# Kernel tuning notes

Hardware: AMD Instinct MI355X
Metric: run time of the kernel (lower is better)

The kernel has to match this reference:

```python
import jax, jax.numpy as jnp
import numpy as np

B, S, D, H = 2, 2048, 1024, 16
A = D // H
NEG = -1e9


def setup_inputs() -> dict:
    key = jax.random.key(0)
    ks = jax.random.split(key, 5)
    std = 1.0 / np.sqrt(D)
    query = jax.random.normal(ks[0], (B, S, D), dtype=jnp.float32)
    context = jax.random.normal(ks[1], (B, S, D), dtype=jnp.float32)
    Wq = jax.random.normal(ks[2], (D, D), dtype=jnp.float32) * std
    Wkv = jax.random.normal(ks[3], (2 * D, D), dtype=jnp.float32) * std
    Wout = jax.random.normal(ks[4], (D, D), dtype=jnp.float32) * std
    # 2D additive causal mask [q_len, c_len]; module broadcasts it over batch and heads
    mask = jnp.where(jnp.tril(jnp.ones((S, S), dtype=bool)), 0.0, NEG).astype(jnp.float32)
    return {"query": query, "context": context, "Wq": Wq, "Wkv": Wkv, "Wout": Wout, "mask": mask}


def reference(query, context, Wq, Wkv, Wout, mask):
    b, q_len, d = query.shape
    c_len = context.shape[1]
    h, a = H, A
    scale = 1.0 / np.sqrt(d)  # NOTE: module scales by 1/sqrt(hidden_dim), not head dim

    q = query @ Wq.T                      # [b, q, d]
    kv = context @ Wkv.T                  # [b, c, 2d]
    k, v = jnp.split(kv, 2, axis=-1)

    q = q.reshape(b, q_len, h, a)
    k = k.reshape(b, c_len, h, a)
    v = v.reshape(b, c_len, h, a)

    scores = jnp.einsum('bqha,bkha->bqkh', q, k)      # [b, q, k, h]
    scores = scores + mask[None, :, :, None]          # mask added BEFORE scaling (faithful)
    attn = jax.nn.softmax(scores * scale, axis=2)     # softmax over key dim
    out = jnp.einsum('bqkh,bkha->bqha', attn, v).reshape(b, q_len, d)
    return out @ Wout.T
```

## Files before the change

### kernel.cpp

```cpp
#include <hip/hip_runtime.h>
#include <hip/hip_bf16.h>
#include <stdint.h>

#define S_LEN 2048
#define DIM   1024
#define NH    16
#define HD    64
#define BATCH 2

typedef __attribute__((ext_vector_type(4))) float f32x4;
typedef __attribute__((ext_vector_type(16))) float f32x16;
typedef __attribute__((ext_vector_type(8))) short bf16x8;
typedef __attribute__((ext_vector_type(4))) int i32x4;
typedef __hip_bfloat16 bf16;

__device__ inline void gload_lds16(const void* g, void* l) {
  __builtin_amdgcn_global_load_lds(
      (const __attribute__((address_space(1))) void*)g,
      (__attribute__((address_space(3))) void*)l, 16, 0, 0);
}

__device__ inline bf16x8 as_bf16x8(i32x4 x) {
  union { i32x4 i; bf16x8 v; } u; u.i = x; return u.v;
}
__device__ inline int cvt_pk_bf16(float lo, float hi) {
  int r;
  asm("v_cvt_pk_bf16_f32 %0, %1, %2" : "=v"(r) : "v"(lo), "v"(hi));
  return r;
}

__global__ __launch_bounds__(256) void cvt_all(
    const float* __restrict__ q, const float* __restrict__ c,
    const float* __restrict__ wq, const float* __restrict__ wkv,
    const float* __restrict__ wo,
    bf16* __restrict__ oq, bf16* __restrict__ oc, bf16* __restrict__ owq,
    bf16* __restrict__ owkv, bf16* __restrict__ owo) {
  const int N0 = 1048576, N1 = 1048576, N2 = 262144, N3 = 524288, N4 = 262144;
  const int total = N0 + N1 + N2 + N3 + N4;
  for (int i = blockIdx.x * 256 + threadIdx.x; i < total; i += gridDim.x * 256) {
    const float* src; bf16* dst; int off = i;
    if (i < N0)                { src = q;   dst = oq; }
    else if (i < N0 + N1)      { src = c;   dst = oc;   off -= N0; }
    else if (i < N0 + N1 + N2) { src = wq;  dst = owq;  off -= N0 + N1; }
    else if (i < N0 + N1 + N2 + N3) { src = wkv; dst = owkv; off -= N0 + N1 + N2; }
    else                       { src = wo;  dst = owo;  off -= N0 + N1 + N2 + N3; }
    float4 v = ((const float4*)src)[off];
    bf16 b0 = __float2bfloat16(v.x), b1 = __float2bfloat16(v.y);
    bf16 b2 = __float2bfloat16(v.z), b3 = __float2bfloat16(v.w);
    ushort4 o;
    o.x = *(unsigned short*)&b0; o.y = *(unsigned short*)&b1;
    o.z = *(unsigned short*)&b2; o.w = *(unsigned short*)&b3;
    ((ushort4*)dst)[off] = o;
  }
}

__device__ inline void gemm128_body(const bf16* __restrict__ A, const bf16* __restrict__ B,
                                    bf16* __restrict__ C, int N, int K, float alpha,
                                    int bm, int bn, bf16* Als, bf16* Bls) {
  const int tid = threadIdx.x;
  const int lane = tid & 63, wid = tid >> 6;
  const int wr = wid >> 1, wc = wid & 1;
  const int fr = lane & 15, fq = lane >> 4;

  f32x4 acc[4][4] = {};
  const int kTiles = K >> 5;
  for (int kt = 0; kt < kTiles; ++kt) {
    const int k0 = kt << 5;
    __syncthreads();
#pragma unroll
    for (int j = 0; j < 2; ++j) {
      int ob = wid * 2048 + j * 1024;
      int o = ob + lane * 16;
      int r = o >> 6;
      int kk = (o & 63) >> 1;
      gload_lds16(A + (size_t)(bm + r) * K + k0 + kk, (char*)Als + ob);
      gload_lds16(B + (size_t)(bn + r) * K + k0 + kk, (char*)Bls + ob);
    }
    __syncthreads();
    bf16x8 af[4], bfr[4];
#pragma unroll
    for (int m = 0; m < 4; ++m)
      af[m] = *(const bf16x8*)(Als + (wr * 64 + m * 16 + fr) * 32 + fq * 8);
#pragma unroll
    for (int n = 0; n < 4; ++n)
      bfr[n] = *(const bf16x8*)(Bls + (wc * 64 + n * 16 + fr) * 32 + fq * 8);
#pragma unroll
    for (int m = 0; m < 4; ++m)
#pragma unroll
      for (int n = 0; n < 4; ++n)
        acc[m][n] = __builtin_amdgcn_mfma_f32_16x16x32_bf16(af[m], bfr[n], acc[m][n], 0, 0, 0);
  }
#pragma unroll
  for (int m = 0; m < 4; ++m)
#pragma unroll
    for (int n = 0; n < 4; ++n)
#pragma unroll
      for (int i = 0; i < 4; ++i) {
        int row = bm + wr * 64 + m * 16 + fq * 4 + i;
        int col = bn + wc * 64 + n * 16 + fr;
        C[(size_t)row * N + col] = __float2bfloat16(acc[m][n][i] * alpha);
      }
}

__global__ __launch_bounds__(256) void gemm_proj(
    const bf16* __restrict__ Aq, const bf16* __restrict__ Bq, bf16* __restrict__ Cq,
    const bf16* __restrict__ Akv, const bf16* __restrict__ Bkv, bf16* __restrict__ Ckv,
    float qalpha) {
  __shared__ __align__(16) bf16 Als[128 * 32];
  __shared__ __align__(16) bf16 Bls[128 * 32];
  const int bid = blockIdx.x;
  const bf16 *A, *B; bf16 *C; int N; float alpha; int bx, by;
  if (bid < 256) { A = Aq;  B = Bq;  C = Cq;  N = 1024; alpha = qalpha; bx = bid & 7;  by = bid >> 3; }
  else { int t = bid - 256; A = Akv; B = Bkv; C = Ckv; N = 2048; alpha = 1.0f; bx = t & 15; by = t >> 4; }
  gemm128_body(A, B, C, N, 1024, alpha, by * 128, bx * 128, Als, Bls);
}

__global__ __launch_bounds__(256) void gemm_bt_n64(
    const bf16* __restrict__ A, const bf16* __restrict__ B,
    float* __restrict__ C, int M, int N, int K) {
  __shared__ __align__(16) bf16 Als[128 * 32];
  __shared__ __align__(16) bf16 Bls[64 * 32];
  const int tid = threadIdx.x;
  const int lane = tid & 63, wid = tid >> 6;
  const int bm = blockIdx.y * 128, bn = blockIdx.x * 64;
  const int fr = lane & 15, fq = lane >> 4;

  f32x4 acc[2][4] = {};
  const int kTiles = K >> 5;
  for (int kt = 0; kt < kTiles; ++kt) {
    const int k0 = kt << 5;
    __syncthreads();
#pragma unroll
    for (int j = 0; j < 2; ++j) {
      int ob = wid * 2048 + j * 1024;
      int o = ob + lane * 16;
      int r = o >> 6;
      int kk = (o & 63) >> 1;
      gload_lds16(A + (size_t)(bm + r) * K + k0 + kk, (char*)Als + ob);
    }
    {
      int ob = wid * 1024;
      int o = ob + lane * 16;
      int r = o >> 6;
      int kk = (o & 63) >> 1;
      gload_lds16(B + (size_t)(bn + r) * K + k0 + kk, (char*)Bls + ob);
    }
    __syncthreads();
    bf16x8 af[2], bfr[4];
#pragma unroll
    for (int m = 0; m < 2; ++m)
      af[m] = *(const bf16x8*)(Als + (wid * 32 + m * 16 + fr) * 32 + fq * 8);
#pragma unroll
    for (int n = 0; n < 4; ++n)
      bfr[n] = *(const bf16x8*)(Bls + (n * 16 + fr) * 32 + fq * 8);
#pragma unroll
    for (int m = 0; m < 2; ++m)
#pragma unroll
      for (int n = 0; n < 4; ++n)
        acc[m][n] = __builtin_amdgcn_mfma_f32_16x16x32_bf16(af[m], bfr[n], acc[m][n], 0, 0, 0);
  }
#pragma unroll
  for (int m = 0; m < 2; ++m)
#pragma unroll
    for (int n = 0; n < 4; ++n)
#pragma unroll
      for (int i = 0; i < 4; ++i) {
        int row = bm + wid * 32 + m * 16 + fq * 4 + i;
        int col = bn + n * 16 + fr;
        C[(size_t)row * N + col] = acc[m][n][i];
      }
}

__global__ __launch_bounds__(256) void transpose_v(
    const bf16* __restrict__ KV, bf16* __restrict__ Vt) {
  __shared__ __align__(16) bf16 tile[64][72];
  const int t = threadIdx.x;
  const int s0 = blockIdx.x * 64, h = blockIdx.y, b = blockIdx.z;
#pragma unroll
  for (int j = 0; j < 2; ++j) {
    int s = j * 32 + (t >> 3);
    int a = (t & 7) * 8;
    bf16x8 v = *(const bf16x8*)(KV + (size_t)(b * S_LEN + s0 + s) * (2 * DIM) + DIM + h * HD + a);
    *(bf16x8*)&tile[s][a] = v;
  }
  __syncthreads();
#pragma unroll
  for (int j = 0; j < 2; ++j) {
    int a = j * 32 + (t >> 3);
    int sc = (t & 7) * 8;
    bf16x8 v;
#pragma unroll
    for (int e = 0; e < 8; ++e)
      ((short*)&v)[e] = *(const short*)&tile[sc + e][a];
    *(bf16x8*)(Vt + (size_t)((b * NH + h) * HD + a) * S_LEN + s0 + sc) = v;
  }
}

__global__ __launch_bounds__(256, 4) void attn_fwd(
    const bf16* __restrict__ Q,
    const bf16* __restrict__ KV,
    const bf16* __restrict__ Vt,
    bf16* __restrict__ O) {
  __shared__ __align__(16) bf16 Kls[3][64 * 64];
  __shared__ __align__(16) bf16 Vls[3][64 * 64];
  __shared__ float Rls[128];
  const int tid = threadIdx.x, lane = tid & 63, wid = tid >> 6;
  const int l31 = lane & 31, hi = lane >> 5;
  const int bid = blockIdx.x;
  const int qx = 15 - (bid >> 5);
  const int hb = bid & 31;
  const int h = hb >> 1, b = hb & 1;
  const int rw0 = qx * 128 + wid * 32;
  const int qrow = rw0 + l31;
  const float NEGINF = -__builtin_inff();

  bf16x8 qf[4];
#pragma unroll
  for (int ka = 0; ka < 4; ++ka)
    qf[ka] = *(const bf16x8*)(Q + (size_t)(b * S_LEN + qrow) * DIM + h * HD + ka * 16 + hi * 8);

  f32x16 oacc[2] = {};
  float rsum = 0.f;

  auto stage = [&](int buf, int kt) {
#pragma unroll
    for (int j = 0; j < 2; ++j) {
      int ob = (wid * 2 + j) * 1024;
      int o = ob + lane * 16;
      int r = o >> 7;
      int sb = (o & 127) ^ ((r & 7) << 4);
      gload_lds16(KV + (size_t)(b * S_LEN + kt * 64 + r) * (2 * DIM) + h * HD + (sb >> 1),
                  (char*)Kls[buf] + ob);
      gload_lds16(Vt + (size_t)((b * NH + h) * HD + r) * S_LEN + kt * 64 + (sb >> 1),
                  (char*)Vls[buf] + ob);
    }
  };

  const int nt = 2 * qx + 2;
  stage(0, 0);
  stage(1, 1 < nt ? 1 : 0);

  for (int kt = 0; kt < nt; ++kt) {
    if (kt + 1 < nt) asm volatile("s_waitcnt vmcnt(4)" ::: "memory");
    else             asm volatile("s_waitcnt vmcnt(0)" ::: "memory");
    __syncthreads();

    const int cb = kt % 3;
    if (64 * kt <= rw0 + 31) {
      const bf16* Kb = Kls[cb];
      const bf16* Vb = Vls[cb];
      const bool maskt = (64 * kt + 63 > rw0);

#pragma unroll
      for (int kb = 0; kb < 2; ++kb) {
        f32x16 c = {};
        __builtin_amdgcn_s_setprio(1);
#pragma unroll
        for (int ka = 0; ka < 4; ++ka) {
          int row = kb * 32 + l31;
          bf16x8 kf = *(const bf16x8*)((const char*)Kb + row * 128 +
                                       ((ka * 32 + hi * 16) ^ ((row & 7) << 4)));
          c = __builtin_amdgcn_mfma_f32_32x32x16_bf16(kf, qf[ka], c, 0, 0, 0);
        }
        __builtin_amdgcn_s_setprio(0);

        float pe[16];
        if (maskt) {
#pragma unroll
          for (int r = 0; r < 16; ++r) {
            int key = kt * 64 + kb * 32 + (r & 3) + 8 * (r >> 2) + 4 * hi;
            float s = (key <= qrow) ? c[r] : NEGINF;
            pe[r] = __builtin_amdgcn_exp2f(s);
            rsum += pe[r];
          }
        } else {
#pragma unroll
          for (int r = 0; r < 16; ++r) {
            pe[r] = __builtin_amdgcn_exp2f(c[r]);
            rsum += pe[r];
          }
        }

        int u[8], x[8];
#pragma unroll
        for (int t = 0; t < 8; ++t) u[t] = cvt_pk_bf16(pe[2 * t], pe[2 * t + 1]);
#pragma unroll
        for (int t = 0; t < 8; ++t) x[t] = __shfl_xor(u[t], 32);
        i32x4 w0, w1;
        w0[0] = hi ? x[2] : u[0]; w0[1] = hi ? x[3] : u[1];
        w0[2] = hi ? u[2] : x[0]; w0[3] = hi ? u[3] : x[1];
        w1[0] = hi ? x[6] : u[4]; w1[1] = hi ? x[7] : u[5];
        w1[2] = hi ? u[6] : x[4]; w1[3] = hi ? u[7] : x[5];
        bf16x8 pa0 = as_bf16x8(w0), pa1 = as_bf16x8(w1);

        __builtin_amdgcn_s_setprio(1);
#pragma unroll
        for (int pl = 0; pl < 2; ++pl) {
          bf16x8 pa = pl ? pa1 : pa0;
#pragma unroll
          for (int nb = 0; nb < 2; ++nb) {
            int a = nb * 32 + l31;
            bf16x8 vf = *(const bf16x8*)((const char*)Vb + a * 128 +
                                         ((kb * 64 + pl * 32 + hi * 16) ^ ((a & 7) << 4)));
            oacc[nb] = __builtin_amdgcn_mfma_f32_32x32x16_bf16(pa, vf, oacc[nb], 0, 0, 0);
          }
        }
        __builtin_amdgcn_s_setprio(0);
      }
    }

    if (kt + 2 < nt) stage((kt + 2) % 3, kt + 2);
  }

  rsum += __shfl_xor(rsum, 32);
  if (hi == 0) Rls[wid * 32 + l31] = 1.0f / rsum;
#pragma unroll
  for (int nb = 0; nb < 2; ++nb)
#pragma unroll
    for (int r = 0; r < 16; ++r) {
      int qloc = (r & 3) + 8 * (r >> 2) + 4 * hi;
      float rv = Rls[wid * 32 + qloc];
      int qg = rw0 + qloc;
      O[(size_t)(b * S_LEN + qg) * DIM + h * HD + nb * 32 + l31] =
          __float2bfloat16(oacc[nb][r] * rv);
    }
}

extern "C" void kernel_launch(void* const* d_in, const int* in_sizes, int n_in,
                              void* d_out, int out_size, void* d_ws, size_t ws_size,
                              hipStream_t stream) {
  (void)in_sizes; (void)n_in; (void)out_size; (void)ws_size;
  const float* query   = (const float*)d_in[0];
  const float* context = (const float*)d_in[1];
  const float* Wq      = (const float*)d_in[2];
  const float* Wkv     = (const float*)d_in[3];
  const float* Wout    = (const float*)d_in[4];
  float* out = (float*)d_out;

  bf16* ws = (bf16*)d_ws;
  const size_t nBSD = (size_t)BATCH * S_LEN * DIM;
  bf16* qbf    = ws;
  bf16* cbf    = qbf + nBSD;
  bf16* wqbf   = cbf + nBSD;
  bf16* wkvbf  = wqbf + (size_t)DIM * DIM;
  bf16* woutbf = wkvbf + (size_t)2 * DIM * DIM;
  bf16* Qp     = woutbf + (size_t)DIM * DIM;
  bf16* KVp    = Qp + nBSD;
  bf16* Vtp    = KVp + 2 * nBSD;
  bf16* Op     = Vtp + nBSD;

  cvt_all<<<2048, 256, 0, stream>>>(query, context, Wq, Wkv, Wout,
                                    qbf, cbf, wqbf, wkvbf, woutbf);

  gemm_proj<<<768, 256, 0, stream>>>(qbf, wqbf, Qp, cbf, wkvbf, KVp, 0.0450842200277801f);

  transpose_v<<<dim3(S_LEN / 64, NH, BATCH), 256, 0, stream>>>(KVp, Vtp);
  attn_fwd<<<512, 256, 0, stream>>>(Qp, KVp, Vtp, Op);
  const int M = BATCH * S_LEN;
  gemm_bt_n64<<<dim3(DIM / 64, M / 128), 256, 0, stream>>>(Op, woutbf, out, M, DIM, DIM);
}
```

Baseline: 126.9 us.

## Split attention key range across two blocks and combine partial outputs

Each causal query tile's key range is split into two halves handled by separate blocks, doubling the grid from 512 to 1024. Unnormalized partial outputs and row sums go to scratch buffers that reuse the already-consumed bf16 input workspace. A new combine kernel sums the two partials and normalizes. This targets load imbalance and low occupancy from the triangular workload, at the cost of an extra launch, extra global traffic, and an extra bf16 rounding of the partials.

```diff
diff --git a/kernel.cpp b/kernel.cpp
--- a/kernel.cpp
+++ b/kernel.cpp
@@ -27,6 +27,11 @@
   int r;
   asm("v_cvt_pk_bf16_f32 %0, %1, %2" : "=v"(r) : "v"(lo), "v"(hi));
   return r;
+}
+__device__ inline float b2f(short s) {
+  union { unsigned int u; float f; } w;
+  w.u = ((unsigned int)(unsigned short)s) << 16;
+  return w.f;
 }
 
 __global__ __launch_bounds__(256) void cvt_all(
@@ -200,27 +205,33 @@
     const bf16* __restrict__ Q,
     const bf16* __restrict__ KV,
     const bf16* __restrict__ Vt,
-    bf16* __restrict__ O) {
+    bf16* __restrict__ Opart,
+    float* __restrict__ Rpart) {
   __shared__ __align__(16) bf16 Kls[3][64 * 64];
   __shared__ __align__(16) bf16 Vls[3][64 * 64];
-  __shared__ float Rls[128];
   const int tid = threadIdx.x, lane = tid & 63, wid = tid >> 6;
   const int l31 = lane & 31, hi = lane >> 5;
   const int bid = blockIdx.x;
-  const int qx = 15 - (bid >> 5);
-  const int hb = bid & 31;
+  const int qx = 15 - (bid >> 6);
+  const int rem = bid & 63;
+  const int c = rem >> 5;
+  const int hb = rem & 31;
   const int h = hb >> 1, b = hb & 1;
   const int rw0 = qx * 128 + wid * 32;
   const int qrow = rw0 + l31;
   const float NEGINF = -__builtin_inff();
 
+  const int cnt = qx + 1;
+  const int kt0 = c * cnt;
+  const int p = ((b * NH + h) * 32) + qx * 2 + c;
+
   bf16x8 qf[4];
 #pragma unroll
   for (int ka = 0; ka < 4; ++ka)
     qf[ka] = *(const bf16x8*)(Q + (size_t)(b * S_LEN + qrow) * DIM + h * HD + ka * 16 + hi * 8);
 
   f32x16 oacc[2] = {};
-  float rsum = 0.f;
+  float rsA[4] = {0.f, 0.f, 0.f, 0.f};
 
   auto stage = [&](int buf, int kt) {
 #pragma unroll
@@ -236,16 +247,16 @@
     }
   };
 
-  const int nt = 2 * qx + 2;
-  stage(0, 0);
-  stage(1, 1 < nt ? 1 : 0);
-
-  for (int kt = 0; kt < nt; ++kt) {
-    if (kt + 1 < nt) asm volatile("s_waitcnt vmcnt(4)" ::: "memory");
+  stage(0, kt0);
+  if (cnt > 1) stage(1, kt0 + 1);
+
+  for (int i = 0; i < cnt; ++i) {
+    const int kt = kt0 + i;
+    if (i + 1 < cnt) asm volatile("s_waitcnt vmcnt(4)" ::: "memory");
     else             asm volatile("s_waitcnt vmcnt(0)" ::: "memory");
     __syncthreads();
 
-    const int cb = kt % 3;
+    const int cb = i % 3;
     if (64 * kt <= rw0 + 31) {
       const bf16* Kb = Kls[cb];
       const bf16* Vb = Vls[cb];
@@ -253,14 +264,14 @@
 
 #pragma unroll
       for (int kb = 0; kb < 2; ++kb) {
-        f32x16 c = {};
+        f32x16 cc = {};
         __builtin_amdgcn_s_setprio(1);
 #pragma unroll
         for (int ka = 0; ka < 4; ++ka) {
           int row = kb * 32 + l31;
           bf16x8 kf = *(const bf16x8*)((const char*)Kb + row * 128 +
                                        ((ka * 32 + hi * 16) ^ ((row & 7) << 4)));
-          c = __builtin_amdgcn_mfma_f32_32x32x16_bf16(kf, qf[ka], c, 0, 0, 0);
+          cc = __builtin_amdgcn_mfma_f32_32x32x16_bf16(kf, qf[ka], cc, 0, 0, 0);
         }
         __builtin_amdgcn_s_setprio(0);
 
@@ -269,15 +280,15 @@
 #pragma unroll
           for (int r = 0; r < 16; ++r) {
             int key = kt * 64 + kb * 32 + (r & 3) + 8 * (r >> 2) + 4 * hi;
-            float s = (key <= qrow) ? c[r] : NEGINF;
+            float s = (key <= qrow) ? cc[r] : NEGINF;
             pe[r] = __builtin_amdgcn_exp2f(s);
-            rsum += pe[r];
+            rsA[r & 3] += pe[r];
           }
         } else {
 #pragma unroll
           for (int r = 0; r < 16; ++r) {
-            pe[r] = __builtin_amdgcn_exp2f(c[r]);
-            rsum += pe[r];
+            pe[r] = __builtin_amdgcn_exp2f(cc[r]);
+            rsA[r & 3] += pe[r];
           }
         }
 
@@ -309,21 +320,47 @@
       }
     }
 
-    if (kt + 2 < nt) stage((kt + 2) % 3, kt + 2);
-  }
-
+    if (i + 2 < cnt) stage((i + 2) % 3, kt0 + i + 2);
+  }
+
+  float rsum = (rsA[0] + rsA[1]) + (rsA[2] + rsA[3]);
   rsum += __shfl_xor(rsum, 32);
-  if (hi == 0) Rls[wid * 32 + l31] = 1.0f / rsum;
+  if (hi == 0) Rpart[p * 128 + wid * 32 + l31] = rsum;
 #pragma unroll
   for (int nb = 0; nb < 2; ++nb)
 #pragma unroll
     for (int r = 0; r < 16; ++r) {
       int qloc = (r & 3) + 8 * (r >> 2) + 4 * hi;
-      float rv = Rls[wid * 32 + qloc];
-      int qg = rw0 + qloc;
-      O[(size_t)(b * S_LEN + qg) * DIM + h * HD + nb * 32 + l31] =
-          __float2bfloat16(oacc[nb][r] * rv);
-    }
+      Opart[(size_t)p * 8192 + (wid * 32 + qloc) * 64 + nb * 32 + l31] =
+          __float2bfloat16(oacc[nb][r]);
+    }
+}
+
+__global__ __launch_bounds__(256) void attn_combine(
+    const bf16* __restrict__ Opart, const float* __restrict__ Rpart,
+    bf16* __restrict__ O) {
+  const int g = blockIdx.x;
+  const int qx = g & 15, bh = g >> 4;
+  const int h = bh & 15, b = bh >> 4;
+  const int t = threadIdx.x;
+  const int row = t >> 1, col0 = (t & 1) * 32;
+  const int p0 = bh * 32 + qx * 2;
+  const size_t o0 = (size_t)p0 * 8192 + row * 64 + col0;
+  const float rinv = 1.0f / (Rpart[p0 * 128 + row] + Rpart[p0 * 128 + 128 + row]);
+  const int s = qx * 128 + row;
+  bf16* dst = O + (size_t)(b * S_LEN + s) * DIM + h * HD + col0;
+#pragma unroll
+  for (int j = 0; j < 4; ++j) {
+    bf16x8 a = *(const bf16x8*)(Opart + o0 + j * 8);
+    bf16x8 cc = *(const bf16x8*)(Opart + o0 + 8192 + j * 8);
+    bf16x8 w;
+#pragma unroll
+    for (int e = 0; e < 8; ++e) {
+      bf16 r = __float2bfloat16((b2f(a[e]) + b2f(cc[e])) * rinv);
+      ((short*)&w)[e] = *(short*)&r;
+    }
+    *(bf16x8*)(dst + j * 8) = w;
+  }
 }
 
 extern "C" void kernel_launch(void* const* d_in, const int* in_sizes, int n_in,
@@ -348,6 +385,8 @@
   bf16* KVp    = Qp + nBSD;
   bf16* Vtp    = KVp + 2 * nBSD;
   bf16* Op     = Vtp + nBSD;
+  bf16*  Opart = qbf;
+  float* Rpart = (float*)wqbf;
 
   cvt_all<<<2048, 256, 0, stream>>>(query, context, Wq, Wkv, Wout,
                                     qbf, cbf, wqbf, wkvbf, woutbf);
@@ -355,7 +394,8 @@
   gemm_proj<<<768, 256, 0, stream>>>(qbf, wqbf, Qp, cbf, wkvbf, KVp, 0.0450842200277801f);
 
   transpose_v<<<dim3(S_LEN / 64, NH, BATCH), 256, 0, stream>>>(KVp, Vtp);
-  attn_fwd<<<512, 256, 0, stream>>>(Qp, KVp, Vtp, Op);
+  attn_fwd<<<1024, 256, 0, stream>>>(Qp, KVp, Vtp, Opart, Rpart);
+  attn_combine<<<512, 256, 0, stream>>>(Opart, Rpart, Op);
   const int M = BATCH * S_LEN;
   gemm_bt_n64<<<dim3(DIM / 64, M / 128), 256, 0, stream>>>(Op, woutbf, out, M, DIM, DIM);
 }
```

Result: faster. 120.4 us (-5.1%).
